# Kernel tuning notes

Measured on AMD Instinct MI355X. Metric: run time of the kernel, lower is better.

Reference implementation:

```python
import jax, jax.numpy as jnp
import numpy as np

N = 100000      # nodes
IN = 256        # in_feats
H = 256         # h_feats
C = 2           # num_classes
E = 400000      # edges per relation
DST_MAX = [70000, 80000, 75000]  # dst ranges -> guarantees isolated nodes per relation


def _build_rel(rng, dst_max):
    """Build one relation: edges, degree mask, induced subgraph on non-isolated nodes."""
    src = rng.integers(0, N, size=E)
    dst = rng.integers(0, dst_max, size=E)
    deg = np.bincount(dst, minlength=N)
    keep = np.where(deg > 0)[0].astype(np.int32)   # nodes with in_degree > 0 (original order)
    iso = np.where(deg == 0)[0].astype(np.int32)   # isolated nodes (original order)
    inv = np.full(N, -1, dtype=np.int64)
    inv[keep] = np.arange(len(keep))
    m = inv[src] >= 0                              # DGL node subgraph keeps edges with both endpoints in set
    ssrc = inv[src[m]].astype(np.int32)
    sdst = inv[dst[m]].astype(np.int32)
    sdeg = np.bincount(sdst, minlength=len(keep))
    norm = (1.0 / np.sqrt(np.clip(sdeg, 1, None))).astype(np.float32)  # D^{-1/2}, clamp(min=1)
    return keep, iso, ssrc, sdst, norm


def setup_inputs() -> dict:
    rng = np.random.default_rng(0)
    key = jax.random.key(0)
    ks = jax.random.split(key, 20)
    d = {"in_feat": jax.random.normal(ks[0], (N, IN), jnp.float32)}
    for r, dm in enumerate(DST_MAX):
        keep, iso, ssrc, sdst, norm = _build_rel(rng, dm)
        d[f"keep{r}"] = jnp.asarray(keep)
        d[f"iso{r}"] = jnp.asarray(iso)
        d[f"src{r}"] = jnp.asarray(ssrc)
        d[f"dst{r}"] = jnp.asarray(sdst)
        d[f"norm{r}"] = jnp.asarray(norm)
        d[f"lam{r}"] = jnp.float32(1.99)  # stand-in for dgl.laplacian_lambda_max (~2 for large graphs)
    s = 0.02
    def W(k, i, o):
        return s * jax.random.normal(k, (i, o), jnp.float32)
    d["W_lin"] = W(ks[1], IN, H);   d["b_lin"] = jnp.zeros((H,), jnp.float32)
    d["W2"]    = W(ks[2], H, H);    d["b2"]    = jnp.zeros((H,), jnp.float32)
    d["W1sg"]  = W(ks[3], H, H);    d["b1sg"]  = jnp.zeros((H,), jnp.float32)
    d["W2sg"]  = W(ks[4], H, H);    d["b2sg"]  = jnp.zeros((H,), jnp.float32)
    d["Wc1"]   = W(ks[5], 2 * H, H); d["bc1"]  = jnp.zeros((H,), jnp.float32)  # ChebConv k=2: Linear(k*H, H)
    d["Wc2"]   = W(ks[6], 2 * H, H); d["bc2"]  = jnp.zeros((H,), jnp.float32)
    d["W3"]    = W(ks[7], 2 * H, H); d["b3"]   = jnp.zeros((H,), jnp.float32)
    d["W4"]    = W(ks[8], H, C);    d["b4"]    = jnp.zeros((C,), jnp.float32)
    return d


def _cheb(x, src, dst, norm, lam, Wc, bc):
    """DGL ChebConv, k=2: X0=x; X1=-re*(D^-.5 A D^-.5 x)+(re-1)*x; relu(Linear([X0,X1]))."""
    re = 2.0 / lam
    xn = x * norm[:, None]
    agg = jax.ops.segment_sum(xn[src], dst, num_segments=x.shape[0]) * norm[:, None]
    X1 = -re * agg + x * (re - 1.0)
    return jax.nn.relu(jnp.concatenate([x, X1], axis=-1) @ Wc + bc)


def reference(in_feat,
              keep0, iso0, src0, dst0, norm0, lam0,
              keep1, iso1, src1, dst1, norm1, lam1,
              keep2, iso2, src2, dst2, norm2, lam2,
              W_lin, b_lin, W2, b2, W1sg, b1sg, W2sg, b2sg,
              Wc1, bc1, Wc2, bc2, W3, b3, W4, b4):
    def block(h, keep, iso, src, dst, norm, lam):
        hk = h[keep]                                   # non-isolated nodes
        h01 = _cheb(hk, src, dst, norm, lam, Wc1, bc1)
        h11 = _cheb(h01, src, dst, norm, lam, Wc2, bc2)
        h02 = h[iso] @ W1sg + b1sg                     # isolated-node branch
        h12 = h02 @ W2sg + b2sg
        h_final = jnp.concatenate([
            jnp.concatenate([h01, h11], axis=-1),      # [M, 2H]
            jnp.concatenate([h02, h12], axis=-1),      # [N-M, 2H]
        ], axis=0)                                     # note: permuted node order, as in original
        return h_final @ W3 + b3

    h = jax.nn.leaky_relu(in_feat @ W_lin + b_lin)
    h = jax.nn.leaky_relu(h @ W2 + b2)
    h_all = []
    rels = [(keep0, iso0, src0, dst0, norm0, lam0),
            (keep1, iso1, src1, dst1, norm1, lam1),
            (keep2, iso2, src2, dst2, norm2, lam2)]
    for rel in rels:
        h = block(h, *rel)   # h is re-used across relations, faithfully to the torch code
        h_all.append(h)
    out = jax.nn.leaky_relu(h_all[0] + h_all[1] + h_all[2])
    return out @ W4 + b4
```

## Files before the change

### kernel.cpp

```cpp
#include <hip/hip_runtime.h>
#include <cstddef>

typedef unsigned short bf16;
typedef short bf16x8 __attribute__((ext_vector_type(8)));
typedef float f32x4 __attribute__((ext_vector_type(4)));
#define LREL 0.01f

__device__ __forceinline__ float bf2f(unsigned int u) {
    union { unsigned int i; float f; } c; c.i = u << 16; return c.f;
}
__device__ __forceinline__ bf16 f2bf(float f) {
    union { unsigned int i; float f; } c; c.f = f;
    return (bf16)((c.i + 0x7FFFu + ((c.i >> 16) & 1u)) >> 16);
}
__device__ __forceinline__ unsigned int pack2(float a, float b) {
    return (unsigned int)f2bf(a) | ((unsigned int)f2bf(b) << 16);
}
__device__ __forceinline__ float activate(float v, int ACT) {
    if (ACT == 1) return v > 0.f ? v : 0.f;
    if (ACT == 2) return v > 0.f ? v : LREL * v;
    return v;
}

template<int ACT, bool DUAL, int ACCMODE, bool GATHER, bool AFP32>
__global__ __launch_bounds__(256) void gemm_mfma(
    const void* __restrict__ A1v, const int* __restrict__ rows1,
    const bf16* __restrict__ A2,
    const bf16* __restrict__ WT1, const bf16* __restrict__ WT2,
    const float* __restrict__ bias,
    bf16* __restrict__ C, bf16* __restrict__ Cacc, int M)
{
    __shared__ bf16 As[128 * 64];
    __shared__ bf16 Bs[256 * 64];
    const int tid  = threadIdx.x;
    const int lane = tid & 63;
    const int wv   = tid >> 6;
    const int row0 = blockIdx.x * 128;

    f32x4 acc[8][4];
#pragma unroll
    for (int mi = 0; mi < 8; ++mi)
#pragma unroll
        for (int ni = 0; ni < 4; ++ni)
#pragma unroll
            for (int e = 0; e < 4; ++e) acc[mi][ni][e] = 0.f;

    const int ar = tid & 127;
    const int ah = tid >> 7;
    const int arow = min(row0 + ar, M - 1);
    const size_t aoff1 = (size_t)(GATHER ? rows1[arow] : arow) * 256;
    const size_t aoff2 = (size_t)arow * 256;

    const int nparts = DUAL ? 2 : 1;
    for (int part = 0; part < nparts; ++part) {
        const bf16* __restrict__ WT = (part == 0) ? WT1 : WT2;
        for (int kt = 0; kt < 256; kt += 64) {
            uint4 areg[4], breg[8];
#pragma unroll
            for (int cc = 0; cc < 4; ++cc) {
                const int c = ah * 4 + cc;
                if (part == 0) {
                    if constexpr (AFP32) {
                        const float* p = (const float*)A1v + aoff1 + kt + c * 8;
                        float4 f0 = *(const float4*)p;
                        float4 f1 = *(const float4*)(p + 4);
                        areg[cc].x = pack2(f0.x, f0.y); areg[cc].y = pack2(f0.z, f0.w);
                        areg[cc].z = pack2(f1.x, f1.y); areg[cc].w = pack2(f1.z, f1.w);
                    } else {
                        areg[cc] = *(const uint4*)((const bf16*)A1v + aoff1 + kt + c * 8);
                    }
                } else {
                    areg[cc] = *(const uint4*)(A2 + aoff2 + kt + c * 8);
                }
            }
#pragma unroll
            for (int cc = 0; cc < 8; ++cc)
                breg[cc] = *(const uint4*)(WT + (size_t)tid * 256 + kt + cc * 8);
            __syncthreads();
#pragma unroll
            for (int cc = 0; cc < 4; ++cc) {
                const int c = ah * 4 + cc;
                *(uint4*)(As + ar * 64 + 8 * (c ^ (ar & 7))) = areg[cc];
            }
#pragma unroll
            for (int cc = 0; cc < 8; ++cc)
                *(uint4*)(Bs + tid * 64 + 8 * (cc ^ (tid & 7))) = breg[cc];
            __syncthreads();
#pragma unroll
            for (int ks = 0; ks < 2; ++ks) {
                const int c = ks * 4 + (lane >> 4);
                bf16x8 bfr[4];
#pragma unroll
                for (int ni = 0; ni < 4; ++ni) {
                    const int n = wv * 64 + ni * 16 + (lane & 15);
                    bfr[ni] = *(const bf16x8*)(Bs + n * 64 + 8 * (c ^ (n & 7)));
                }
#pragma unroll
                for (int mi = 0; mi < 8; ++mi) {
                    const int r = mi * 16 + (lane & 15);
                    bf16x8 af = *(const bf16x8*)(As + r * 64 + 8 * (c ^ (r & 7)));
#pragma unroll
                    for (int ni = 0; ni < 4; ++ni)
                        acc[mi][ni] = __builtin_amdgcn_mfma_f32_16x16x32_bf16(
                            bfr[ni], af, acc[mi][ni], 0, 0, 0);
                }
            }
        }
    }

#pragma unroll
    for (int mi = 0; mi < 8; ++mi) {
        const int r = row0 + mi * 16 + (lane & 15);
        if (r < M) {
#pragma unroll
            for (int ni = 0; ni < 4; ++ni) {
                const int c0 = wv * 64 + ni * 16 + (lane >> 4) * 4;
                float o[4];
#pragma unroll
                for (int reg = 0; reg < 4; ++reg)
                    o[reg] = activate(acc[mi][ni][reg] + bias[c0 + reg], ACT);
                uint2 cv; cv.x = pack2(o[0], o[1]); cv.y = pack2(o[2], o[3]);
                *(uint2*)(C + (size_t)r * 256 + c0) = cv;
                if constexpr (ACCMODE == 1) {
                    *(uint2*)(Cacc + (size_t)r * 256 + c0) = cv;
                } else if constexpr (ACCMODE == 2) {
                    uint2 ov = *(const uint2*)(Cacc + (size_t)r * 256 + c0);
                    uint2 nv2;
                    nv2.x = pack2(bf2f(ov.x & 0xFFFFu) + o[0], bf2f(ov.x >> 16) + o[1]);
                    nv2.y = pack2(bf2f(ov.y & 0xFFFFu) + o[2], bf2f(ov.y >> 16) + o[3]);
                    *(uint2*)(Cacc + (size_t)r * 256 + c0) = nv2;
                }
            }
        }
    }
}

__global__ void wconv_all(const float* __restrict__ W_lin, const float* __restrict__ W2,
                          const float* __restrict__ W1sg, const float* __restrict__ W2sg,
                          const float* __restrict__ Wc1, const float* __restrict__ Wc2,
                          const float* __restrict__ W3, bf16* __restrict__ out)
{
    const int b = blockIdx.x;
    const int m = b >> 8, k = b & 255, n = threadIdx.x;
    const float* src;
    switch (m) {
        case 0: src = W_lin; break;       case 1: src = W2; break;
        case 2: src = W1sg; break;        case 3: src = W2sg; break;
        case 4: src = Wc1; break;         case 5: src = Wc1 + 65536; break;
        case 6: src = Wc2; break;         case 7: src = Wc2 + 65536; break;
        case 8: src = W3; break;          default: src = W3 + 65536; break;
    }
    out[(size_t)m * 65536 + n * 256 + k] = f2bf(src[k * 256 + n]);
}

template<bool GATHER>
__global__ void agg_x1(const bf16* __restrict__ x, const int* __restrict__ gidx,
                       const float* __restrict__ norm,
                       const int* __restrict__ rp, const int* __restrict__ ssrc,
                       const float* __restrict__ lam, bf16* __restrict__ X1, int M)
{
    int d = blockIdx.x * 4 + (threadIdx.x >> 6);
    if (d >= M) return;
    int l = threadIdx.x & 63;
    float s0 = 0.f, s1 = 0.f, s2 = 0.f, s3 = 0.f;
    int e0 = rp[d], e1 = rp[d + 1];
    for (int e = e0; e < e1; ++e) {
        int si = ssrc[e];
        float nv = norm[si];
        const bf16* xr = x + (size_t)(GATHER ? gidx[si] : si) * 256 + l * 4;
        uint2 u = *(const uint2*)xr;
        s0 += bf2f(u.x & 0xFFFFu) * nv; s1 += bf2f(u.x >> 16) * nv;
        s2 += bf2f(u.y & 0xFFFFu) * nv; s3 += bf2f(u.y >> 16) * nv;
    }
    float re = 2.0f / lam[0];
    float a = -re * norm[d];
    float b = re - 1.0f;
    const bf16* xdp = x + (size_t)(GATHER ? gidx[d] : d) * 256 + l * 4;
    uint2 xd = *(const uint2*)xdp;
    uint2 o;
    o.x = pack2(a * s0 + b * bf2f(xd.x & 0xFFFFu), a * s1 + b * bf2f(xd.x >> 16));
    o.y = pack2(a * s2 + b * bf2f(xd.y & 0xFFFFu), a * s3 + b * bf2f(xd.y >> 16));
    *(uint2*)(X1 + (size_t)d * 256 + l * 4) = o;
}

__global__ void zero_k(int* __restrict__ p, int n)
{
    int i = blockIdx.x * 256 + threadIdx.x;
    if (i < n) p[i] = 0;
}

__global__ void hist_k(const int* __restrict__ dst, int* __restrict__ deg, int E)
{
    int e = blockIdx.x * 256 + threadIdx.x;
    if (e < E) atomicAdd(&deg[dst[e]], 1);
}

__global__ void scan1_k(const int* __restrict__ deg, int* __restrict__ bsum, int M)
{
    __shared__ int red[256];
    int b = blockIdx.x, t = threadIdx.x;
    int base = b * 1024 + t * 4;
    int s = 0;
#pragma unroll
    for (int j = 0; j < 4; ++j) { int i = base + j; if (i < M) s += deg[i]; }
    red[t] = s; __syncthreads();
    for (int off = 128; off; off >>= 1) {
        if (t < off) red[t] += red[t + off];
        __syncthreads();
    }
    if (t == 0) bsum[b] = red[0];
}
__global__ void scan2_k(int* __restrict__ bsum, int nb, int* __restrict__ rp, int M)
{
    __shared__ int buf[256];
    int t = threadIdx.x;
    int v = (t < nb) ? bsum[t] : 0;
    buf[t] = v; __syncthreads();
    for (int off = 1; off < 256; off <<= 1) {
        int y = (t >= off) ? buf[t - off] : 0;
        __syncthreads();
        buf[t] += y;
        __syncthreads();
    }
    if (t < nb) bsum[t] = buf[t] - v;
    if (t == 0) rp[M] = buf[255];
}
__global__ void scan3_k(const int* __restrict__ deg, const int* __restrict__ bsum,
                        int* __restrict__ rp, int M)
{
    __shared__ int buf[256];
    int b = blockIdx.x, t = threadIdx.x;
    int base = b * 1024 + t * 4;
    int v0 = (base + 0 < M) ? deg[base + 0] : 0;
    int v1 = (base + 1 < M) ? deg[base + 1] : 0;
    int v2 = (base + 2 < M) ? deg[base + 2] : 0;
    int v3 = (base + 3 < M) ? deg[base + 3] : 0;
    int s = v0 + v1 + v2 + v3;
    buf[t] = s; __syncthreads();
    for (int off = 1; off < 256; off <<= 1) {
        int y = (t >= off) ? buf[t - off] : 0;
        __syncthreads();
        buf[t] += y;
        __syncthreads();
    }
    int ex = bsum[b] + buf[t] - s;
    if (base + 0 < M) rp[base + 0] = ex;
    if (base + 1 < M) rp[base + 1] = ex + v0;
    if (base + 2 < M) rp[base + 2] = ex + v0 + v1;
    if (base + 3 < M) rp[base + 3] = ex + v0 + v1 + v2;
}

__global__ void scatter_k(const int* __restrict__ src, const int* __restrict__ dst,
                          const int* __restrict__ rp, int* __restrict__ cursor,
                          int* __restrict__ out, int E)
{
    int e = blockIdx.x * 256 + threadIdx.x;
    if (e < E) {
        int d = dst[e];
        int pos = rp[d] + atomicAdd(&cursor[d], 1);
        out[pos] = src[e];
    }
}

__global__ void final_k(const bf16* __restrict__ acc, const float* __restrict__ W4,
                        const float* __restrict__ b4, float* __restrict__ out, int Nn)
{
    int r = blockIdx.x * 4 + (threadIdx.x >> 6);
    if (r >= Nn) return;
    int l = threadIdx.x & 63;
    uint2 u = *(const uint2*)(acc + (size_t)r * 256 + l * 4);
    float v[4] = { bf2f(u.x & 0xFFFFu), bf2f(u.x >> 16),
                   bf2f(u.y & 0xFFFFu), bf2f(u.y >> 16) };
    float s0 = 0.f, s1 = 0.f;
#pragma unroll
    for (int j = 0; j < 4; ++j) {
        float x = v[j] > 0.f ? v[j] : LREL * v[j];
        int k = l * 4 + j;
        s0 += x * W4[k * 2 + 0];
        s1 += x * W4[k * 2 + 1];
    }
#pragma unroll
    for (int off = 32; off; off >>= 1) {
        s0 += __shfl_xor(s0, off, 64);
        s1 += __shfl_xor(s1, off, 64);
    }
    if (l == 0) {
        out[(size_t)r * 2 + 0] = s0 + b4[0];
        out[(size_t)r * 2 + 1] = s1 + b4[1];
    }
}

extern "C" void kernel_launch(void* const* d_in, const int* in_sizes, int n_in,
                              void* d_out, int out_size, void* d_ws, size_t ws_size,
                              hipStream_t stream)
{
    const float* in_feat = (const float*)d_in[0];
    const int Nn = in_sizes[0] / 256;

    const float* W_lin = (const float*)d_in[19]; const float* b_lin = (const float*)d_in[20];
    const float* W2p   = (const float*)d_in[21]; const float* b2   = (const float*)d_in[22];
    const float* W1sg  = (const float*)d_in[23]; const float* b1sg = (const float*)d_in[24];
    const float* W2sg  = (const float*)d_in[25]; const float* b2sg = (const float*)d_in[26];
    const float* Wc1   = (const float*)d_in[27]; const float* bc1  = (const float*)d_in[28];
    const float* Wc2   = (const float*)d_in[29]; const float* bc2  = (const float*)d_in[30];
    const float* W3p   = (const float*)d_in[31]; const float* b3   = (const float*)d_in[32];
    const float* W4p   = (const float*)d_in[33]; const float* b4   = (const float*)d_in[34];

    int Mr[3], NIr[3], Er[3];
    int M_max = 0, NI_max = 0, E_max = 0;
    for (int r = 0; r < 3; ++r) {
        Mr[r]  = in_sizes[1 + 6 * r];
        NIr[r] = in_sizes[2 + 6 * r];
        Er[r]  = in_sizes[3 + 6 * r];
        if (Mr[r] > M_max)  M_max  = Mr[r];
        if (NIr[r] > NI_max) NI_max = NIr[r];
        if (Er[r] > E_max)  E_max  = Er[r];
    }

    bf16* ACC = (bf16*)d_ws;
    bf16* H   = ACC + (size_t)Nn * 256;
    bf16* S1  = H + (size_t)Nn * 256;
    bf16* S2  = S1 + (size_t)M_max * 256;
    bf16* S3  = S2 + (size_t)M_max * 256;
    bf16* S4  = S3 + (size_t)M_max * 256;
    bf16* WTb = S4 + (size_t)NI_max * 256;
    int* deg    = (int*)(WTb + 10 * 65536);
    int* cursor = deg + (Nn + 1);
    int* rp     = cursor + (Nn + 1);
    int* bsum   = rp + (Nn + 1);
    int* ssrc   = bsum + 256;

    bf16* WT_lin = WTb;             bf16* WT_2   = WTb + 1 * 65536;
    bf16* WT_1sg = WTb + 2 * 65536; bf16* WT_2sg = WTb + 3 * 65536;
    bf16* WT_c1a = WTb + 4 * 65536; bf16* WT_c1b = WTb + 5 * 65536;
    bf16* WT_c2a = WTb + 6 * 65536; bf16* WT_c2b = WTb + 7 * 65536;
    bf16* WT_3a  = WTb + 8 * 65536; bf16* WT_3b  = WTb + 9 * 65536;

    auto g1 = [](int M) { return dim3((unsigned)((M + 127) / 128)); };

    wconv_all<<<2560, 256, 0, stream>>>(W_lin, W2p, W1sg, W2sg, Wc1, Wc2, W3p, WTb);

    gemm_mfma<2, false, 0, false, true><<<g1(Nn), 256, 0, stream>>>(
        in_feat, nullptr, nullptr, WT_lin, nullptr, b_lin, ACC, nullptr, Nn);
    gemm_mfma<2, false, 0, false, false><<<g1(Nn), 256, 0, stream>>>(
        ACC, nullptr, nullptr, WT_2, nullptr, b2, H, nullptr, Nn);

    for (int r = 0; r < 3; ++r) {
        const int*   keep = (const int*)d_in[1 + 6 * r];
        const int*   iso  = (const int*)d_in[2 + 6 * r];
        const int*   srcA = (const int*)d_in[3 + 6 * r];
        const int*   dstA = (const int*)d_in[4 + 6 * r];
        const float* norm = (const float*)d_in[5 + 6 * r];
        const float* lam  = (const float*)d_in[6 + 6 * r];
        const int M  = Mr[r];
        const int NI = NIr[r];
        const int E  = Er[r];
        const int nb = (M + 1023) / 1024;

        zero_k<<<(2 * (Nn + 1) + 255) / 256, 256, 0, stream>>>(deg, 2 * (Nn + 1));
        hist_k<<<(E + 255) / 256, 256, 0, stream>>>(dstA, deg, E);
        scan1_k<<<nb, 256, 0, stream>>>(deg, bsum, M);
        scan2_k<<<1, 256, 0, stream>>>(bsum, nb, rp, M);
        scan3_k<<<nb, 256, 0, stream>>>(deg, bsum, rp, M);
        scatter_k<<<(E + 255) / 256, 256, 0, stream>>>(srcA, dstA, rp, cursor, ssrc, E);

        agg_x1<true><<<(M + 3) / 4, 256, 0, stream>>>(H, keep, norm, rp, ssrc, lam, S1, M);
        gemm_mfma<1, true, 0, true, false><<<g1(M), 256, 0, stream>>>(
            H, keep, S1, WT_c1a, WT_c1b, bc1, S2, nullptr, M);
        agg_x1<false><<<(M + 3) / 4, 256, 0, stream>>>(S2, nullptr, norm, rp, ssrc, lam, S1, M);
        gemm_mfma<1, true, 0, false, false><<<g1(M), 256, 0, stream>>>(
            S2, nullptr, S1, WT_c2a, WT_c2b, bc2, S3, nullptr, M);

        gemm_mfma<0, false, 0, true, false><<<g1(NI), 256, 0, stream>>>(
            H, iso, nullptr, WT_1sg, nullptr, b1sg, S1, nullptr, NI);
        gemm_mfma<0, false, 0, false, false><<<g1(NI), 256, 0, stream>>>(
            S1, nullptr, nullptr, WT_2sg, nullptr, b2sg, S4, nullptr, NI);

        if (r == 0) {
            gemm_mfma<0, true, 1, false, false><<<g1(NI), 256, 0, stream>>>(
                S1, nullptr, S4, WT_3a, WT_3b, b3,
                H + (size_t)M * 256, ACC + (size_t)M * 256, NI);
            gemm_mfma<0, true, 1, false, false><<<g1(M), 256, 0, stream>>>(
                S2, nullptr, S3, WT_3a, WT_3b, b3, H, ACC, M);
        } else {
            gemm_mfma<0, true, 2, false, false><<<g1(NI), 256, 0, stream>>>(
                S1, nullptr, S4, WT_3a, WT_3b, b3,
                H + (size_t)M * 256, ACC + (size_t)M * 256, NI);
            gemm_mfma<0, true, 2, false, false><<<g1(M), 256, 0, stream>>>(
                S2, nullptr, S3, WT_3a, WT_3b, b3, H, ACC, M);
        }
    }

    final_k<<<(Nn + 3) / 4, 256, 0, stream>>>(ACC, W4p, b4, (float*)d_out, Nn);
}
```

Measured before the change: 2.476 ms.

## Use 512-thread GEMM blocks with register prefetch and LDS-staged coalesced epilogue

Rewrites the MFMA GEMM kernel to use 8 waves per block, each owning 32 output columns instead of 64, which halves the accumulator registers per thread and is meant to raise occupancy. Global loads for the next K step are issued into registers before the current step's MFMAs run, so memory latency can overlap with compute. The epilogue stages each 16-row tile through LDS and writes 16-byte coalesced rows, including the accumulate path. The cost is extra barriers per tile in the epilogue and launch bounds that may force register limits.

```diff
diff --git a/kernel.cpp b/kernel.cpp
--- a/kernel.cpp
+++ b/kernel.cpp
@@ -23,7 +23,7 @@
 }
 
 template<int ACT, bool DUAL, int ACCMODE, bool GATHER, bool AFP32>
-__global__ __launch_bounds__(256) void gemm_mfma(
+__global__ __launch_bounds__(512, 4) void gemm_mfma(
     const void* __restrict__ A1v, const int* __restrict__ rows1,
     const bf16* __restrict__ A2,
     const bf16* __restrict__ WT1, const bf16* __restrict__ WT2,
@@ -34,14 +34,14 @@
     __shared__ bf16 Bs[256 * 64];
     const int tid  = threadIdx.x;
     const int lane = tid & 63;
-    const int wv   = tid >> 6;
+    const int w    = tid >> 6;
     const int row0 = blockIdx.x * 128;
 
-    f32x4 acc[8][4];
+    f32x4 acc[8][2];
 #pragma unroll
     for (int mi = 0; mi < 8; ++mi)
 #pragma unroll
-        for (int ni = 0; ni < 4; ++ni)
+        for (int ni = 0; ni < 2; ++ni)
 #pragma unroll
             for (int e = 0; e < 4; ++e) acc[mi][ni][e] = 0.f;
 
@@ -50,86 +50,111 @@
     const int arow = min(row0 + ar, M - 1);
     const size_t aoff1 = (size_t)(GATHER ? rows1[arow] : arow) * 256;
     const size_t aoff2 = (size_t)arow * 256;
-
-    const int nparts = DUAL ? 2 : 1;
-    for (int part = 0; part < nparts; ++part) {
-        const bf16* __restrict__ WT = (part == 0) ? WT1 : WT2;
-        for (int kt = 0; kt < 256; kt += 64) {
-            uint4 areg[4], breg[8];
-#pragma unroll
-            for (int cc = 0; cc < 4; ++cc) {
-                const int c = ah * 4 + cc;
-                if (part == 0) {
-                    if constexpr (AFP32) {
-                        const float* p = (const float*)A1v + aoff1 + kt + c * 8;
-                        float4 f0 = *(const float4*)p;
-                        float4 f1 = *(const float4*)(p + 4);
-                        areg[cc].x = pack2(f0.x, f0.y); areg[cc].y = pack2(f0.z, f0.w);
-                        areg[cc].z = pack2(f1.x, f1.y); areg[cc].w = pack2(f1.z, f1.w);
-                    } else {
-                        areg[cc] = *(const uint4*)((const bf16*)A1v + aoff1 + kt + c * 8);
-                    }
+    const int bn = tid & 255;
+    const int bh = tid >> 8;
+
+    const int nsteps = DUAL ? 8 : 4;
+    uint4 aprf[2], bprf[4];
+
+    auto loadStep = [&](int s) {
+        const int part = DUAL ? (s >> 2) : 0;
+        const int kt = (s & 3) * 64;
+#pragma unroll
+        for (int cc = 0; cc < 2; ++cc) {
+            const int c = ah * 2 + cc;
+            if (part == 0) {
+                if constexpr (AFP32) {
+                    const float* p = (const float*)A1v + aoff1 + kt + c * 8;
+                    float4 f0 = *(const float4*)p;
+                    float4 f1 = *(const float4*)(p + 4);
+                    aprf[cc].x = pack2(f0.x, f0.y); aprf[cc].y = pack2(f0.z, f0.w);
+                    aprf[cc].z = pack2(f1.x, f1.y); aprf[cc].w = pack2(f1.z, f1.w);
                 } else {
-                    areg[cc] = *(const uint4*)(A2 + aoff2 + kt + c * 8);
+                    aprf[cc] = *(const uint4*)((const bf16*)A1v + aoff1 + kt + c * 8);
                 }
+            } else {
+                aprf[cc] = *(const uint4*)(A2 + aoff2 + kt + c * 8);
             }
-#pragma unroll
-            for (int cc = 0; cc < 8; ++cc)
-                breg[cc] = *(const uint4*)(WT + (size_t)tid * 256 + kt + cc * 8);
-            __syncthreads();
-#pragma unroll
-            for (int cc = 0; cc < 4; ++cc) {
-                const int c = ah * 4 + cc;
-                *(uint4*)(As + ar * 64 + 8 * (c ^ (ar & 7))) = areg[cc];
+        }
+        const bf16* __restrict__ WT = (DUAL && (s >> 2)) ? WT2 : WT1;
+#pragma unroll
+        for (int cc = 0; cc < 4; ++cc) {
+            const int c = bh * 4 + cc;
+            bprf[cc] = *(const uint4*)(WT + (size_t)bn * 256 + kt + c * 8);
+        }
+    };
+
+    loadStep(0);
+    for (int s = 0; s < nsteps; ++s) {
+        __syncthreads();
+#pragma unroll
+        for (int cc = 0; cc < 2; ++cc) {
+            const int c = ah * 2 + cc;
+            *(uint4*)(As + ar * 64 + 8 * (c ^ (ar & 7))) = aprf[cc];
+        }
+#pragma unroll
+        for (int cc = 0; cc < 4; ++cc) {
+            const int c = bh * 4 + cc;
+            *(uint4*)(Bs + bn * 64 + 8 * (c ^ (bn & 7))) = bprf[cc];
+        }
+        __syncthreads();
+        if (s + 1 < nsteps) loadStep(s + 1);
+#pragma unroll
+        for (int ks = 0; ks < 2; ++ks) {
+            const int c = ks * 4 + (lane >> 4);
+            bf16x8 bfr[2];
+#pragma unroll
+            for (int ni = 0; ni < 2; ++ni) {
+                const int n = w * 32 + ni * 16 + (lane & 15);
+                bfr[ni] = *(const bf16x8*)(Bs + n * 64 + 8 * (c ^ (n & 7)));
             }
 #pragma unroll
-            for (int cc = 0; cc < 8; ++cc)
-                *(uint4*)(Bs + tid * 64 + 8 * (cc ^ (tid & 7))) = breg[cc];
-            __syncthreads();
-#pragma unroll
-            for (int ks = 0; ks < 2; ++ks) {
-                const int c = ks * 4 + (lane >> 4);
-                bf16x8 bfr[4];
-#pragma unroll
-                for (int ni = 0; ni < 4; ++ni) {
-                    const int n = wv * 64 + ni * 16 + (lane & 15);
-                    bfr[ni] = *(const bf16x8*)(Bs + n * 64 + 8 * (c ^ (n & 7)));
-                }
-#pragma unroll
-                for (int mi = 0; mi < 8; ++mi) {
-                    const int r = mi * 16 + (lane & 15);
-                    bf16x8 af = *(const bf16x8*)(As + r * 64 + 8 * (c ^ (r & 7)));
-#pragma unroll
-                    for (int ni = 0; ni < 4; ++ni)
-                        acc[mi][ni] = __builtin_amdgcn_mfma_f32_16x16x32_bf16(
-                            bfr[ni], af, acc[mi][ni], 0, 0, 0);
-                }
+            for (int mi = 0; mi < 8; ++mi) {
+                const int r = mi * 16 + (lane & 15);
+                bf16x8 af = *(const bf16x8*)(As + r * 64 + 8 * (c ^ (r & 7)));
+#pragma unroll
+                for (int ni = 0; ni < 2; ++ni)
+                    acc[mi][ni] = __builtin_amdgcn_mfma_f32_16x16x32_bf16(
+                        bfr[ni], af, acc[mi][ni], 0, 0, 0);
             }
         }
     }
 
-#pragma unroll
+    bf16* T = As;
+    const int m = lane & 15;
+    const int rr = tid >> 5;
+    const int ch = tid & 31;
     for (int mi = 0; mi < 8; ++mi) {
-        const int r = row0 + mi * 16 + (lane & 15);
+        __syncthreads();
+#pragma unroll
+        for (int ni = 0; ni < 2; ++ni) {
+            const int n0 = w * 32 + ni * 16 + (lane >> 4) * 4;
+            float o0 = activate(acc[mi][ni][0] + bias[n0 + 0], ACT);
+            float o1 = activate(acc[mi][ni][1] + bias[n0 + 1], ACT);
+            float o2 = activate(acc[mi][ni][2] + bias[n0 + 2], ACT);
+            float o3 = activate(acc[mi][ni][3] + bias[n0 + 3], ACT);
+            *(unsigned int*)(T + m * 264 + n0)     = pack2(o0, o1);
+            *(unsigned int*)(T + m * 264 + n0 + 2) = pack2(o2, o3);
+        }
+        __syncthreads();
+        const int r = row0 + mi * 16 + rr;
         if (r < M) {
-#pragma unroll
-            for (int ni = 0; ni < 4; ++ni) {
-                const int c0 = wv * 64 + ni * 16 + (lane >> 4) * 4;
-                float o[4];
-#pragma unroll
-                for (int reg = 0; reg < 4; ++reg)
-                    o[reg] = activate(acc[mi][ni][reg] + bias[c0 + reg], ACT);
-                uint2 cv; cv.x = pack2(o[0], o[1]); cv.y = pack2(o[2], o[3]);
-                *(uint2*)(C + (size_t)r * 256 + c0) = cv;
-                if constexpr (ACCMODE == 1) {
-                    *(uint2*)(Cacc + (size_t)r * 256 + c0) = cv;
-                } else if constexpr (ACCMODE == 2) {
-                    uint2 ov = *(const uint2*)(Cacc + (size_t)r * 256 + c0);
-                    uint2 nv2;
-                    nv2.x = pack2(bf2f(ov.x & 0xFFFFu) + o[0], bf2f(ov.x >> 16) + o[1]);
-                    nv2.y = pack2(bf2f(ov.y & 0xFFFFu) + o[2], bf2f(ov.y >> 16) + o[3]);
-                    *(uint2*)(Cacc + (size_t)r * 256 + c0) = nv2;
-                }
+            uint4 v = *(const uint4*)(T + rr * 264 + ch * 8);
+            *(uint4*)(C + (size_t)r * 256 + ch * 8) = v;
+            if constexpr (ACCMODE == 1) {
+                *(uint4*)(Cacc + (size_t)r * 256 + ch * 8) = v;
+            } else if constexpr (ACCMODE == 2) {
+                uint4 ov = *(const uint4*)(Cacc + (size_t)r * 256 + ch * 8);
+                uint4 nv;
+                nv.x = pack2(bf2f(ov.x & 0xFFFFu) + bf2f(v.x & 0xFFFFu),
+                             bf2f(ov.x >> 16)     + bf2f(v.x >> 16));
+                nv.y = pack2(bf2f(ov.y & 0xFFFFu) + bf2f(v.y & 0xFFFFu),
+                             bf2f(ov.y >> 16)     + bf2f(v.y >> 16));
+                nv.z = pack2(bf2f(ov.z & 0xFFFFu) + bf2f(v.z & 0xFFFFu),
+                             bf2f(ov.z >> 16)     + bf2f(v.z >> 16));
+                nv.w = pack2(bf2f(ov.w & 0xFFFFu) + bf2f(v.w & 0xFFFFu),
+                             bf2f(ov.w >> 16)     + bf2f(v.w >> 16));
+                *(uint4*)(Cacc + (size_t)r * 256 + ch * 8) = nv;
             }
         }
     }
@@ -340,9 +365,9 @@
 
     wconv_all<<<2560, 256, 0, stream>>>(W_lin, W2p, W1sg, W2sg, Wc1, Wc2, W3p, WTb);
 
-    gemm_mfma<2, false, 0, false, true><<<g1(Nn), 256, 0, stream>>>(
+    gemm_mfma<2, false, 0, false, true><<<g1(Nn), 512, 0, stream>>>(
         in_feat, nullptr, nullptr, WT_lin, nullptr, b_lin, ACC, nullptr, Nn);
-    gemm_mfma<2, false, 0, false, false><<<g1(Nn), 256, 0, stream>>>(
+    gemm_mfma<2, false, 0, false, false><<<g1(Nn), 512, 0, stream>>>(
         ACC, nullptr, nullptr, WT_2, nullptr, b2, H, nullptr, Nn);
 
     for (int r = 0; r < 3; ++r) {
@@ -365,28 +390,28 @@
         scatter_k<<<(E + 255) / 256, 256, 0, stream>>>(srcA, dstA, rp, cursor, ssrc, E);
 
         agg_x1<true><<<(M + 3) / 4, 256, 0, stream>>>(H, keep, norm, rp, ssrc, lam, S1, M);
-        gemm_mfma<1, true, 0, true, false><<<g1(M), 256, 0, stream>>>(
+        gemm_mfma<1, true, 0, true, false><<<g1(M), 512, 0, stream>>>(
             H, keep, S1, WT_c1a, WT_c1b, bc1, S2, nullptr, M);
         agg_x1<false><<<(M + 3) / 4, 256, 0, stream>>>(S2, nullptr, norm, rp, ssrc, lam, S1, M);
-        gemm_mfma<1, true, 0, false, false><<<g1(M), 256, 0, stream>>>(
+        gemm_mfma<1, true, 0, false, false><<<g1(M), 512, 0, stream>>>(
             S2, nullptr, S1, WT_c2a, WT_c2b, bc2, S3, nullptr, M);
 
-        gemm_mfma<0, false, 0, true, false><<<g1(NI), 256, 0, stream>>>(
+        gemm_mfma<0, false, 0, true, false><<<g1(NI), 512, 0, stream>>>(
             H, iso, nullptr, WT_1sg, nullptr, b1sg, S1, nullptr, NI);
-        gemm_mfma<0, false, 0, false, false><<<g1(NI), 256, 0, stream>>>(
+        gemm_mfma<0, false, 0, false, false><<<g1(NI), 512, 0, stream>>>(
             S1, nullptr, nullptr, WT_2sg, nullptr, b2sg, S4, nullptr, NI);
 
         if (r == 0) {
-            gemm_mfma<0, true, 1, false, false><<<g1(NI), 256, 0, stream>>>(
+            gemm_mfma<0, true, 1, false, false><<<g1(NI), 512, 0, stream>>>(
                 S1, nullptr, S4, WT_3a, WT_3b, b3,
                 H + (size_t)M * 256, ACC + (size_t)M * 256, NI);
-            gemm_mfma<0, true, 1, false, false><<<g1(M), 256, 0, stream>>>(
+            gemm_mfma<0, true, 1, false, false><<<g1(M), 512, 0, stream>>>(
                 S2, nullptr, S3, WT_3a, WT_3b, b3, H, ACC, M);
         } else {
-            gemm_mfma<0, true, 2, false, false><<<g1(NI), 256, 0, stream>>>(
+            gemm_mfma<0, true, 2, false, false><<<g1(NI), 512, 0, stream>>>(
                 S1, nullptr, S4, WT_3a, WT_3b, b3,
                 H + (size_t)M * 256, ACC + (size_t)M * 256, NI);
-            gemm_mfma<0, true, 2, false, false><<<g1(M), 256, 0, stream>>>(
+            gemm_mfma<0, true, 2, false, false><<<g1(M), 512, 0, stream>>>(
                 S2, nullptr, S3, WT_3a, WT_3b, b3, H, ACC, M);
         }
     }
```

Result: faster. 2.172 ms (-12.3%).
